# Performance work log

Measured on AMD Instinct MI355X. Metric: run time of the kernel, lower is better.

The kernel has to match this reference:

```python
import jax, jax.numpy as jnp
import numpy as np

CF_ITERS = 5
CF_K = 0.02
DECAY = [0.9, 0.93, 0.85, 0.97, 0.88, 0.94]
N_CHAMBERS = 6
RES_DIM = 100
B = 262144

COUPLING = np.array([
    [0.0, -0.3, 0.6, 0.4, -0.2, 0.3],
    [-0.3, 0.0, -0.5, -0.7, 0.6, 0.4],
    [0.6, -0.5, 0.0, 0.3, -0.3, 0.2],
    [0.4, -0.7, 0.3, 0.0, -0.4, 0.5],
    [-0.2, 0.6, -0.3, -0.4, 0.0, 0.3],
    [0.3, 0.4, 0.2, 0.5, 0.3, 0.0]], dtype=np.float32)


def _init_linear(key, c, fan_out, fan_in):
    kw, kb = jax.random.split(key)
    bound = 1.0 / np.sqrt(fan_in)
    W = jax.random.uniform(kw, (c, fan_out, fan_in), jnp.float32, -bound, bound)
    b = jax.random.uniform(kb, (c, fan_out), jnp.float32, -bound, bound)
    return W, b


def setup_inputs() -> dict:
    key = jax.random.key(0)
    ks = jax.random.split(key, 5)
    res = jax.random.normal(ks[0], (B, RES_DIM), jnp.float32)
    W1, b1 = _init_linear(ks[1], N_CHAMBERS, 128, RES_DIM)
    W2, b2 = _init_linear(ks[2], N_CHAMBERS, 64, 128)
    W3, b3 = _init_linear(ks[3], N_CHAMBERS, 32, 64)
    W4, b4 = _init_linear(ks[4], N_CHAMBERS, 1, 32)
    coupling = jnp.asarray(COUPLING)
    return {"res": res, "W1": W1, "b1": b1, "W2": W2, "b2": b2,
            "W3": W3, "b3": b3, "W4": W4, "b4": b4, "coupling": coupling}


def reference(res, W1, b1, W2, b2, W3, b3, W4, b4, coupling):
    silu = jax.nn.silu
    # batched 6 per-chamber MLPs: [B, C, hidden]
    h = silu(jnp.einsum('bd,chd->bch', res, W1) + b1)      # [B,6,128]
    h = silu(jnp.einsum('bch,coh->bco', h, W2) + b2)       # [B,6,64]
    h = silu(jnp.einsum('bco,cpo->bcp', h, W3) + b3)       # [B,6,32]
    raw = (jnp.einsum('bcp,cqp->bcq', h, W4) + b4)[..., 0]  # [B,6]
    act = jax.nn.sigmoid(raw)
    decay = jnp.asarray(DECAY, dtype=jnp.float32)
    for _ in range(CF_ITERS):
        act = act * decay
        # infl[b,i,j] = CF_K * sin(act[b,j] - act[b,i])
        infl = CF_K * jnp.sin(act[:, None, :] - act[:, :, None])  # [B,6,6]
        act = act + jnp.sum(infl * coupling[None], axis=2)
        act = jnp.clip(act, 0.0, 1.0)
    return (act, raw)
```

## Files before the change

kernel.cpp:

```cpp
#include <hip/hip_runtime.h>


typedef unsigned int u32;
typedef __attribute__((ext_vector_type(8))) short bf16x8;
typedef __attribute__((ext_vector_type(4))) float f32x4;

#define RES_DIM 100
#define NCH 6
#define FRAGS_PER_CH 52
#define NFRAG (NCH*FRAGS_PER_CH)
#define WS_BYTES ((size_t)NFRAG*2048)

#define MFMA16 __builtin_amdgcn_mfma_f32_16x16x32_bf16
#define CFENCE() asm volatile("" ::: "memory")

union FragU { bf16x8 v; u32 u[4]; uint4 q; };

__device__ __forceinline__ void split2(float f0, float f1, u32 &hp, u32 &lp){
    u32 h;
    asm("v_cvt_pk_bf16_f32 %0, %1, %2" : "=v"(h) : "v"(f0), "v"(f1));
    float l0 = f0 - __uint_as_float(h << 16);
    float l1 = f1 - __uint_as_float(h & 0xffff0000u);
    u32 l;
    asm("v_cvt_pk_bf16_f32 %0, %1, %2" : "=v"(l) : "v"(l0), "v"(l1));
    hp = h; lp = l;
}

__device__ __forceinline__ float silu1(float x){
    return x * __builtin_amdgcn_rcpf(1.f + __expf(-x));
}
__device__ __forceinline__ f32x4 silu4(f32x4 v){
    f32x4 r; r[0]=silu1(v[0]); r[1]=silu1(v[1]); r[2]=silu1(v[2]); r[3]=silu1(v[3]); return r;
}
__device__ __forceinline__ float sin_rev(float x){ return __builtin_amdgcn_sinf(x*0.15915494309189535f); }

__device__ __forceinline__ void load_frag(const u32* __restrict__ wsb, int frag, int lane,
                                          bf16x8 &h, bf16x8 &l){
    const uint4* p = (const uint4*)(wsb + ((size_t)frag << 9) + (lane << 3));
    FragU H, L; H.q = p[0]; L.q = p[1];
    h = H.v; l = L.v;
}

__device__ __forceinline__ f32x4 triple(f32x4 acc, bf16x8 ah, bf16x8 al, bf16x8 bh, bf16x8 bl){
    acc = MFMA16(ah, bh, acc, 0, 0, 0);
    acc = MFMA16(al, bh, acc, 0, 0, 0);
    acc = MFMA16(ah, bl, acc, 0, 0, 0);
    return acc;
}

__global__ void __launch_bounds__(256) prep_kernel(
    const float* __restrict__ W1, const float* __restrict__ W2,
    const float* __restrict__ W3, u32* __restrict__ ws)
{
    const int f = blockIdx.x * 4 + (threadIdx.x >> 6);
    const int lane = threadIdx.x & 63;
    const int c = f / FRAGS_PER_CH, r = f % FRAGS_PER_CH;
    const int n15 = lane & 15, quad = lane >> 4;
    float vals[8];
    if (r < 32) {
        int n = r >> 2, k = r & 3;
        const float* wp = W1 + (size_t)c*128*RES_DIM + (size_t)(n*16 + n15)*RES_DIM;
        #pragma unroll
        for (int j=0;j<8;j++){
            int kk = k*32 + quad*8 + j;
            vals[j] = (kk < RES_DIM) ? wp[kk] : 0.f;
        }
    } else if (r < 48) {
        int rr = r - 32; int n = rr >> 2, k = rr & 3;
        const float* wp = W2 + (size_t)c*64*128 + (size_t)(n*16 + n15)*128;
        #pragma unroll
        for (int j=0;j<8;j++) vals[j] = wp[k*32 + quad*8 + j];
    } else {
        int rr = r - 48; int n = rr >> 1, k = rr & 1;
        const float* wp = W3 + (size_t)c*32*64 + (size_t)(n*16 + n15)*64;
        #pragma unroll
        for (int j=0;j<8;j++) vals[j] = wp[k*32 + quad*8 + j];
    }
    u32 hp[4], lp[4];
    #pragma unroll
    for (int i=0;i<4;i++) split2(vals[2*i], vals[2*i+1], hp[i], lp[i]);
    u32* dst = ws + ((size_t)f << 9) + (lane << 3);
    *(uint4*)(dst)     = make_uint4(hp[0],hp[1],hp[2],hp[3]);
    *(uint4*)(dst + 4) = make_uint4(lp[0],lp[1],lp[2],lp[3]);
}

#define TB_STRIDE 36
#define TB_SIZE (32*TB_STRIDE)

__global__ void __launch_bounds__(256, 2) chambers_mfma(
    const float* __restrict__ res, const u32* __restrict__ wsb,
    const float* __restrict__ b1, const float* __restrict__ b2,
    const float* __restrict__ b3, const float* __restrict__ W4,
    const float* __restrict__ b4, const float* __restrict__ Cpl,
    float* __restrict__ out, int nsamp)
{
    __shared__ __align__(16) float tb[4][TB_SIZE];
    __shared__ float rawld[4*32*7];

    const int tid  = threadIdx.x;
    const int w    = tid >> 6, lane = tid & 63;
    const int n15  = lane & 15, quad = lane >> 4;
    const int m_base = (blockIdx.x * 4 + w) * 32;

    bf16x8 rh[2][4], rl[2][4];
    #pragma unroll
    for (int mt=0; mt<2; mt++){
        const float* row = res + (size_t)(m_base + mt*16 + n15) * RES_DIM;
        #pragma unroll
        for (int ks=0; ks<4; ks++){
            float v[8];
            if (ks < 3){
                float4 A = *(const float4*)(row + ks*32 + quad*8);
                float4 B = *(const float4*)(row + ks*32 + quad*8 + 4);
                v[0]=A.x; v[1]=A.y; v[2]=A.z; v[3]=A.w;
                v[4]=B.x; v[5]=B.y; v[6]=B.z; v[7]=B.w;
            } else {
                float4 A = make_float4(0.f,0.f,0.f,0.f);
                if (quad == 0) A = *(const float4*)(row + 96);
                v[0]=A.x; v[1]=A.y; v[2]=A.z; v[3]=A.w;
                v[4]=0.f; v[5]=0.f; v[6]=0.f; v[7]=0.f;
            }
            FragU H, L;
            #pragma unroll
            for (int i=0;i<4;i++) split2(v[2*i], v[2*i+1], H.u[i], L.u[i]);
            rh[mt][ks]=H.v; rl[mt][ks]=L.v;
        }
    }

    for (int c=0; c<NCH; c++){
        const float* b1c = b1 + c*128;
        const float* b2c = b2 + c*64;
        const float* b3c = b3 + c*32;
        const int fbase = c*FRAGS_PER_CH;

        f32x4 c2[2][4];
        #pragma unroll
        for (int mt=0; mt<2; mt++)
            #pragma unroll
            for (int nt=0; nt<4; nt++){
                float bb = b2c[nt*16 + n15];
                f32x4 t = {bb,bb,bb,bb}; c2[mt][nt] = t;
            }

        bf16x8 fh[4], fl[4];
        load_frag(wsb, fbase + 0, lane, fh[0], fl[0]);
        load_frag(wsb, fbase + 1, lane, fh[1], fl[1]);
        load_frag(wsb, fbase + 2, lane, fh[2], fl[2]);
        load_frag(wsb, fbase + 3, lane, fh[3], fl[3]);

        for (int kk=0; kk<4; kk++){
            bf16x8 w2h[4], w2l[4];
            #pragma unroll
            for (int nt=0; nt<4; nt++) load_frag(wsb, fbase + 32 + nt*4 + kk, lane, w2h[nt], w2l[nt]);

            #pragma unroll
            for (int pp=0; pp<2; pp++){
                int p = kk*2 + pp;
                float bb = b1c[p*16 + n15];
                f32x4 z = {0.f,0.f,0.f,0.f};
                f32x4 A0h = {bb,bb,bb,bb}, A0u = z, A0v = z;
                f32x4 A1h = A0h,           A1u = z, A1v = z;
                #pragma unroll
                for (int ks=0; ks<4; ks++){
                    bf16x8 bh = fh[ks], bl = fl[ks];
                    if (p*4 + ks < 28)
                        load_frag(wsb, fbase + p*4 + ks + 4, lane, fh[ks], fl[ks]);
                    A0h = MFMA16(rh[0][ks], bh, A0h, 0,0,0);
                    A1h = MFMA16(rh[1][ks], bh, A1h, 0,0,0);
                    A0u = MFMA16(rl[0][ks], bh, A0u, 0,0,0);
                    A1u = MFMA16(rl[1][ks], bh, A1u, 0,0,0);
                    A0v = MFMA16(rh[0][ks], bl, A0v, 0,0,0);
                    A1v = MFMA16(rh[1][ks], bl, A1v, 0,0,0);
                }
                f32x4 s0 = silu4((A0h + A0u) + A0v);
                f32x4 s1 = silu4((A1h + A1u) + A1v);
                #pragma unroll
                for (int r=0; r<4; r++){
                    tb[w][(quad*4 + r)*TB_STRIDE      + pp*16 + n15] = s0[r];
                    tb[w][(16 + quad*4 + r)*TB_STRIDE + pp*16 + n15] = s1[r];
                }
            }
            CFENCE();
            bf16x8 a2h[2], a2l[2];
            #pragma unroll
            for (int mt=0; mt<2; mt++){
                const float* qp = &tb[w][(mt*16 + n15)*TB_STRIDE + quad*8];
                float4 A = *(const float4*)qp;
                float4 B = *(const float4*)(qp + 4);
                FragU H, L;
                split2(A.x, A.y, H.u[0], L.u[0]);
                split2(A.z, A.w, H.u[1], L.u[1]);
                split2(B.x, B.y, H.u[2], L.u[2]);
                split2(B.z, B.w, H.u[3], L.u[3]);
                a2h[mt]=H.v; a2l[mt]=L.v;
            }
            CFENCE();
            #pragma unroll
            for (int nt=0; nt<4; nt++){
                c2[0][nt] = triple(c2[0][nt], a2h[0], a2l[0], w2h[nt], w2l[nt]);
                c2[1][nt] = triple(c2[1][nt], a2h[1], a2l[1], w2h[nt], w2l[nt]);
            }
        }
        #pragma unroll
        for (int mt=0; mt<2; mt++)
            #pragma unroll
            for (int nt=0; nt<4; nt++) c2[mt][nt] = silu4(c2[mt][nt]);

        f32x4 c3[2][2];
        #pragma unroll
        for (int mt=0; mt<2; mt++)
            #pragma unroll
            for (int nt=0; nt<2; nt++){
                float bb = b3c[nt*16 + n15];
                f32x4 t = {bb,bb,bb,bb}; c3[mt][nt] = t;
            }
        for (int k3=0; k3<2; k3++){
            bf16x8 w3h[2], w3l[2];
            #pragma unroll
            for (int nt=0; nt<2; nt++) load_frag(wsb, fbase + 48 + nt*2 + k3, lane, w3h[nt], w3l[nt]);
            #pragma unroll
            for (int mt=0; mt<2; mt++)
                #pragma unroll
                for (int q2=0; q2<2; q2++)
                    #pragma unroll
                    for (int r=0; r<4; r++)
                        tb[w][(mt*16 + quad*4 + r)*TB_STRIDE + q2*16 + n15] = c2[mt][2*k3+q2][r];
            CFENCE();
            bf16x8 a3h[2], a3l[2];
            #pragma unroll
            for (int mt=0; mt<2; mt++){
                const float* qp = &tb[w][(mt*16 + n15)*TB_STRIDE + quad*8];
                float4 A = *(const float4*)qp;
                float4 B = *(const float4*)(qp + 4);
                FragU H, L;
                split2(A.x, A.y, H.u[0], L.u[0]);
                split2(A.z, A.w, H.u[1], L.u[1]);
                split2(B.x, B.y, H.u[2], L.u[2]);
                split2(B.z, B.w, H.u[3], L.u[3]);
                a3h[mt]=H.v; a3l[mt]=L.v;
            }
            CFENCE();
            #pragma unroll
            for (int nt=0; nt<2; nt++){
                c3[0][nt] = triple(c3[0][nt], a3h[0], a3l[0], w3h[nt], w3l[nt]);
                c3[1][nt] = triple(c3[1][nt], a3h[1], a3l[1], w3h[nt], w3l[nt]);
            }
        }
        #pragma unroll
        for (int mt=0; mt<2; mt++)
            #pragma unroll
            for (int nt=0; nt<2; nt++) c3[mt][nt] = silu4(c3[mt][nt]);

        float w4a = W4[c*32 + n15];
        float w4b = W4[c*32 + 16 + n15];
        float bb4 = b4[c];
        #pragma unroll
        for (int mt=0; mt<2; mt++){
            float t0 = c3[mt][0][0]*w4a + c3[mt][1][0]*w4b;
            float t1 = c3[mt][0][1]*w4a + c3[mt][1][1]*w4b;
            float t2 = c3[mt][0][2]*w4a + c3[mt][1][2]*w4b;
            float t3 = c3[mt][0][3]*w4a + c3[mt][1][3]*w4b;
            #pragma unroll
            for (int off=1; off<16; off<<=1){
                t0 += __shfl_xor(t0, off, 64);
                t1 += __shfl_xor(t1, off, 64);
                t2 += __shfl_xor(t2, off, 64);
                t3 += __shfl_xor(t3, off, 64);
            }
            if (n15 == 0){
                int mb = w*32 + mt*16 + quad*4;
                rawld[(mb+0)*7 + c] = t0 + bb4;
                rawld[(mb+1)*7 + c] = t1 + bb4;
                rawld[(mb+2)*7 + c] = t2 + bb4;
                rawld[(mb+3)*7 + c] = t3 + bb4;
            }
        }
    }
    __threadfence_block();

    const int m = lane & 31;
    float rw[6], a[6];
    #pragma unroll
    for (int j=0;j<6;j++){
        rw[j] = rawld[(w*32 + m)*7 + j];
        a[j]  = __builtin_amdgcn_rcpf(1.f + __expf(-rw[j]));
    }
    const float dec[6] = {0.9f,0.93f,0.85f,0.97f,0.88f,0.94f};
    float C[6][6];
    #pragma unroll
    for (int i=0;i<6;i++)
        #pragma unroll
        for (int j=0;j<6;j++) C[i][j] = Cpl[i*6+j];
    #pragma unroll
    for (int it=0; it<5; it++){
        #pragma unroll
        for (int j=0;j<6;j++) a[j] *= dec[j];
        float nz[6];
        #pragma unroll
        for (int i=0;i<6;i++){
            float sum = 0.f;
            #pragma unroll
            for (int j=0;j<6;j++) sum += sin_rev(a[j]-a[i]) * C[i][j];
            nz[i] = a[i] + 0.02f*sum;
        }
        #pragma unroll
        for (int i=0;i<6;i++) a[i] = fminf(fmaxf(nz[i],0.f),1.f);
    }
    if (lane < 32){
        size_t s = (size_t)m_base + m;
        #pragma unroll
        for (int j=0;j<6;j++) out[s*6 + j] = a[j];
        size_t rb = (size_t)nsamp*6 + s*6;
        #pragma unroll
        for (int j=0;j<6;j++) out[rb + j] = rw[j];
    }
}

__global__ void __launch_bounds__(256, 2) chambers_fb(
    const float* __restrict__ res, const float* __restrict__ W1, const float* __restrict__ b1,
    const float* __restrict__ W2, const float* __restrict__ b2,
    const float* __restrict__ W3, const float* __restrict__ b3,
    const float* __restrict__ W4, const float* __restrict__ b4,
    const float* __restrict__ Cpl, float* __restrict__ out, int nsamp)
{
    __shared__ float w2t[128*64];
    __shared__ float h3buf[256][33];
    __shared__ float rawbuf[256][7];
    const int tid = threadIdx.x;
    const long long s = (long long)blockIdx.x * 256 + tid;
    float rf[RES_DIM];
    {
        const float4* rp = (const float4*)(res + s*RES_DIM);
        #pragma unroll
        for (int i=0;i<25;i++){
            float4 v = rp[i];
            rf[4*i+0]=v.x; rf[4*i+1]=v.y; rf[4*i+2]=v.z; rf[4*i+3]=v.w;
        }
    }
    for (int c=0;c<6;c++){
        __syncthreads();
        {
            const float* w2c = W2 + c*64*128;
            for (int k=tid; k<64*128; k+=256){
                int o = k >> 7, u = k & 127;
                w2t[u*64 + o] = w2c[k];
            }
        }
        __syncthreads();
        const float* w1c = W1 + c*128*RES_DIM;
        const float* b1c = b1 + c*128;
        const float* b2c = b2 + c*64;
        float h2a[64];
        #pragma unroll
        for (int o=0;o<64;o++) h2a[o] = b2c[o];
        for (int u=0; u<128; u+=2){
            const float4* wa = (const float4*)(w1c + u*RES_DIM);
            const float4* wb = wa + 25;
            float a0=0.f,a1=0.f,a2=0.f,a3=0.f;
            #pragma unroll
            for (int i=0;i<25;i++){
                float4 va=wa[i], vb=wb[i];
                a0 = fmaf(va.x, rf[4*i+0], a0); a0 = fmaf(va.y, rf[4*i+1], a0);
                a2 = fmaf(va.z, rf[4*i+2], a2); a2 = fmaf(va.w, rf[4*i+3], a2);
                a1 = fmaf(vb.x, rf[4*i+0], a1); a1 = fmaf(vb.y, rf[4*i+1], a1);
                a3 = fmaf(vb.z, rf[4*i+2], a3); a3 = fmaf(vb.w, rf[4*i+3], a3);
            }
            float hh0 = silu1(a0+a2+b1c[u]);
            float hh1 = silu1(a1+a3+b1c[u+1]);
            const float* wr0 = &w2t[u*64];
            const float* wr1 = &w2t[(u+1)*64];
            #pragma unroll
            for (int o=0;o<64;o+=4){
                float4 va = *(const float4*)(wr0+o);
                float4 vb = *(const float4*)(wr1+o);
                h2a[o+0] = fmaf(va.x, hh0, fmaf(vb.x, hh1, h2a[o+0]));
                h2a[o+1] = fmaf(va.y, hh0, fmaf(vb.y, hh1, h2a[o+1]));
                h2a[o+2] = fmaf(va.z, hh0, fmaf(vb.z, hh1, h2a[o+2]));
                h2a[o+3] = fmaf(va.w, hh0, fmaf(vb.w, hh1, h2a[o+3]));
            }
        }
        #pragma unroll
        for (int o=0;o<64;o++) h2a[o] = silu1(h2a[o]);
        {
            const float* w3c = W3 + c*32*64;
            const float* b3c = b3 + c*32;
            for (int p=0; p<32; p+=2){
                const float4* wa = (const float4*)(w3c + p*64);
                const float4* wb = wa + 16;
                float a0=0.f,a1=0.f,a2=0.f,a3=0.f;
                #pragma unroll
                for (int k=0;k<16;k++){
                    float4 va=wa[k], vb=wb[k];
                    a0 = fmaf(va.x, h2a[4*k+0], a0); a0 = fmaf(va.y, h2a[4*k+1], a0);
                    a2 = fmaf(va.z, h2a[4*k+2], a2); a2 = fmaf(va.w, h2a[4*k+3], a2);
                    a1 = fmaf(vb.x, h2a[4*k+0], a1); a1 = fmaf(vb.y, h2a[4*k+1], a1);
                    a3 = fmaf(vb.z, h2a[4*k+2], a3); a3 = fmaf(vb.w, h2a[4*k+3], a3);
                }
                h3buf[tid][p]   = silu1(a0+a2+b3c[p]);
                h3buf[tid][p+1] = silu1(a1+a3+b3c[p+1]);
            }
        }
        {
            const float4* w4p = (const float4*)(W4 + c*32);
            float a0=0.f, a1=0.f;
            #pragma unroll
            for (int k=0;k<8;k++){
                float4 v = w4p[k];
                a0 = fmaf(v.x, h3buf[tid][4*k+0], a0);
                a1 = fmaf(v.y, h3buf[tid][4*k+1], a1);
                a0 = fmaf(v.z, h3buf[tid][4*k+2], a0);
                a1 = fmaf(v.w, h3buf[tid][4*k+3], a1);
            }
            rawbuf[tid][c] = a0+a1+b4[c];
        }
    }
    float a[6], rw[6];
    #pragma unroll
    for (int j=0;j<6;j++){ rw[j]=rawbuf[tid][j]; a[j]=__builtin_amdgcn_rcpf(1.f+__expf(-rw[j])); }
    const float dec[6] = {0.9f,0.93f,0.85f,0.97f,0.88f,0.94f};
    float C[6][6];
    #pragma unroll
    for (int i=0;i<6;i++)
        #pragma unroll
        for (int j=0;j<6;j++) C[i][j]=Cpl[i*6+j];
    #pragma unroll
    for (int it=0; it<5; it++){
        #pragma unroll
        for (int j=0;j<6;j++) a[j]*=dec[j];
        float nz[6];
        #pragma unroll
        for (int i=0;i<6;i++){
            float sum=0.f;
            #pragma unroll
            for (int j=0;j<6;j++) sum += sin_rev(a[j]-a[i]) * C[i][j];
            nz[i]=a[i]+0.02f*sum;
        }
        #pragma unroll
        for (int i=0;i<6;i++) a[i]=fminf(fmaxf(nz[i],0.f),1.f);
    }
    long long ob = s*6;
    #pragma unroll
    for (int j=0;j<6;j++) out[ob+j] = a[j];
    long long rb = (long long)nsamp*6 + ob;
    #pragma unroll
    for (int j=0;j<6;j++) out[rb+j] = rw[j];
}

extern "C" void kernel_launch(void* const* d_in, const int* in_sizes, int n_in,
                              void* d_out, int out_size, void* d_ws, size_t ws_size,
                              hipStream_t stream) {
    const float* res = (const float*)d_in[0];
    const float* W1  = (const float*)d_in[1];
    const float* b1  = (const float*)d_in[2];
    const float* W2  = (const float*)d_in[3];
    const float* b2  = (const float*)d_in[4];
    const float* W3  = (const float*)d_in[5];
    const float* b3  = (const float*)d_in[6];
    const float* W4  = (const float*)d_in[7];
    const float* b4  = (const float*)d_in[8];
    const float* Cpl = (const float*)d_in[9];
    float* out = (float*)d_out;
    int nsamp = in_sizes[0] / RES_DIM;

    if (ws_size >= WS_BYTES) {
        u32* ws = (u32*)d_ws;
        prep_kernel<<<NFRAG/4, 256, 0, stream>>>(W1, W2, W3, ws);
        chambers_mfma<<<nsamp/128, 256, 0, stream>>>(res, ws, b1, b2, b3, W4, b4, Cpl, out, nsamp);
    } else {
        chambers_fb<<<nsamp/256, 256, 0, stream>>>(res, W1, b1, W2, b2, W3, b3, W4, b4, Cpl, out, nsamp);
    }
}
```

Baseline: 421.3 us.

## Switch layer-1 GEMM to 32x32x16 MFMA with K=112 padding

```diff
diff --git a/kernel.cpp b/kernel.cpp
--- a/kernel.cpp
+++ b/kernel.cpp
@@ -4,14 +4,16 @@
 typedef unsigned int u32;
 typedef __attribute__((ext_vector_type(8))) short bf16x8;
 typedef __attribute__((ext_vector_type(4))) float f32x4;
+typedef __attribute__((ext_vector_type(16))) float f32x16;
 
 #define RES_DIM 100
 #define NCH 6
-#define FRAGS_PER_CH 52
+#define FRAGS_PER_CH 48
 #define NFRAG (NCH*FRAGS_PER_CH)
 #define WS_BYTES ((size_t)NFRAG*2048)
 
 #define MFMA16 __builtin_amdgcn_mfma_f32_16x16x32_bf16
+#define MFMA32 __builtin_amdgcn_mfma_f32_32x32x16_bf16
 #define CFENCE() asm volatile("" ::: "memory")
 
 union FragU { bf16x8 v; u32 u[4]; uint4 q; };
@@ -57,21 +59,22 @@
     const int c = f / FRAGS_PER_CH, r = f % FRAGS_PER_CH;
     const int n15 = lane & 15, quad = lane >> 4;
     float vals[8];
-    if (r < 32) {
-        int n = r >> 2, k = r & 3;
-        const float* wp = W1 + (size_t)c*128*RES_DIM + (size_t)(n*16 + n15)*RES_DIM;
+    if (r < 28) {
+        int nt = r / 7, ks7 = r % 7;
+        const float* wp = W1 + (size_t)c*128*RES_DIM + (size_t)(nt*32 + (lane & 31))*RES_DIM;
+        int kb = ks7*16 + (lane >> 5)*8;
         #pragma unroll
         for (int j=0;j<8;j++){
-            int kk = k*32 + quad*8 + j;
+            int kk = kb + j;
             vals[j] = (kk < RES_DIM) ? wp[kk] : 0.f;
         }
-    } else if (r < 48) {
-        int rr = r - 32; int n = rr >> 2, k = rr & 3;
+    } else if (r < 44) {
+        int rr = r - 28; int n = rr >> 2, k = rr & 3;
         const float* wp = W2 + (size_t)c*64*128 + (size_t)(n*16 + n15)*128;
         #pragma unroll
         for (int j=0;j<8;j++) vals[j] = wp[k*32 + quad*8 + j];
     } else {
-        int rr = r - 48; int n = rr >> 1, k = rr & 1;
+        int rr = r - 44; int n = rr >> 1, k = rr & 1;
         const float* wp = W3 + (size_t)c*32*64 + (size_t)(n*16 + n15)*64;
         #pragma unroll
         for (int j=0;j<8;j++) vals[j] = wp[k*32 + quad*8 + j];
@@ -100,30 +103,31 @@
     const int tid  = threadIdx.x;
     const int w    = tid >> 6, lane = tid & 63;
     const int n15  = lane & 15, quad = lane >> 4;
+    const int n31  = lane & 31, h32 = lane >> 5;
     const int m_base = (blockIdx.x * 4 + w) * 32;
 
-    bf16x8 rh[2][4], rl[2][4];
-    #pragma unroll
-    for (int mt=0; mt<2; mt++){
-        const float* row = res + (size_t)(m_base + mt*16 + n15) * RES_DIM;
-        #pragma unroll
-        for (int ks=0; ks<4; ks++){
+    bf16x8 rAh[7], rAl[7];
+    {
+        const float* row = res + (size_t)(m_base + n31) * RES_DIM;
+        #pragma unroll
+        for (int ks7=0; ks7<7; ks7++){
+            int kb = ks7*16 + h32*8;
             float v[8];
-            if (ks < 3){
-                float4 A = *(const float4*)(row + ks*32 + quad*8);
-                float4 B = *(const float4*)(row + ks*32 + quad*8 + 4);
+            if (ks7 < 6){
+                float4 A = *(const float4*)(row + kb);
+                float4 B = *(const float4*)(row + kb + 4);
                 v[0]=A.x; v[1]=A.y; v[2]=A.z; v[3]=A.w;
                 v[4]=B.x; v[5]=B.y; v[6]=B.z; v[7]=B.w;
             } else {
                 float4 A = make_float4(0.f,0.f,0.f,0.f);
-                if (quad == 0) A = *(const float4*)(row + 96);
+                if (h32 == 0) A = *(const float4*)(row + 96);
                 v[0]=A.x; v[1]=A.y; v[2]=A.z; v[3]=A.w;
                 v[4]=0.f; v[5]=0.f; v[6]=0.f; v[7]=0.f;
             }
             FragU H, L;
             #pragma unroll
             for (int i=0;i<4;i++) split2(v[2*i], v[2*i+1], H.u[i], L.u[i]);
-            rh[mt][ks]=H.v; rl[mt][ks]=L.v;
+            rAh[ks7]=H.v; rAl[ks7]=L.v;
         }
     }
 
@@ -142,43 +146,34 @@
                 f32x4 t = {bb,bb,bb,bb}; c2[mt][nt] = t;
             }
 
-        bf16x8 fh[4], fl[4];
+        bf16x8 fh[2], fl[2];
         load_frag(wsb, fbase + 0, lane, fh[0], fl[0]);
         load_frag(wsb, fbase + 1, lane, fh[1], fl[1]);
-        load_frag(wsb, fbase + 2, lane, fh[2], fl[2]);
-        load_frag(wsb, fbase + 3, lane, fh[3], fl[3]);
-
+
+        #pragma unroll
         for (int kk=0; kk<4; kk++){
             bf16x8 w2h[4], w2l[4];
             #pragma unroll
-            for (int nt=0; nt<4; nt++) load_frag(wsb, fbase + 32 + nt*4 + kk, lane, w2h[nt], w2l[nt]);
-
-            #pragma unroll
-            for (int pp=0; pp<2; pp++){
-                int p = kk*2 + pp;
-                float bb = b1c[p*16 + n15];
-                f32x4 z = {0.f,0.f,0.f,0.f};
-                f32x4 A0h = {bb,bb,bb,bb}, A0u = z, A0v = z;
-                f32x4 A1h = A0h,           A1u = z, A1v = z;
-                #pragma unroll
-                for (int ks=0; ks<4; ks++){
-                    bf16x8 bh = fh[ks], bl = fl[ks];
-                    if (p*4 + ks < 28)
-                        load_frag(wsb, fbase + p*4 + ks + 4, lane, fh[ks], fl[ks]);
-                    A0h = MFMA16(rh[0][ks], bh, A0h, 0,0,0);
-                    A1h = MFMA16(rh[1][ks], bh, A1h, 0,0,0);
-                    A0u = MFMA16(rl[0][ks], bh, A0u, 0,0,0);
-                    A1u = MFMA16(rl[1][ks], bh, A1u, 0,0,0);
-                    A0v = MFMA16(rh[0][ks], bl, A0v, 0,0,0);
-                    A1v = MFMA16(rh[1][ks], bl, A1v, 0,0,0);
-                }
-                f32x4 s0 = silu4((A0h + A0u) + A0v);
-                f32x4 s1 = silu4((A1h + A1u) + A1v);
-                #pragma unroll
-                for (int r=0; r<4; r++){
-                    tb[w][(quad*4 + r)*TB_STRIDE      + pp*16 + n15] = s0[r];
-                    tb[w][(16 + quad*4 + r)*TB_STRIDE + pp*16 + n15] = s1[r];
-                }
+            for (int nt=0; nt<4; nt++) load_frag(wsb, fbase + 28 + nt*4 + kk, lane, w2h[nt], w2l[nt]);
+
+            float bb = b1c[kk*32 + n31];
+            f32x16 Dh, Dc1, Dc2;
+            #pragma unroll
+            for (int i=0;i<16;i++){ Dh[i]=bb; Dc1[i]=0.f; Dc2[i]=0.f; }
+            #pragma unroll
+            for (int ks7=0; ks7<7; ks7++){
+                const int i = kk*7 + ks7;
+                bf16x8 bh = fh[i & 1], bl = fl[i & 1];
+                if (i < 26) load_frag(wsb, fbase + i + 2, lane, fh[i & 1], fl[i & 1]);
+                Dh  = MFMA32(rAh[ks7], bh, Dh,  0,0,0);
+                Dc1 = MFMA32(rAl[ks7], bh, Dc1, 0,0,0);
+                Dc2 = MFMA32(rAh[ks7], bl, Dc2, 0,0,0);
+            }
+            #pragma unroll
+            for (int reg=0; reg<16; reg++){
+                float d = silu1((Dh[reg] + Dc1[reg]) + Dc2[reg]);
+                int m = (reg & 3) + 8*(reg >> 2) + 4*h32;
+                tb[w][m*TB_STRIDE + n31] = d;
             }
             CFENCE();
             bf16x8 a2h[2], a2l[2];
@@ -217,7 +212,7 @@
         for (int k3=0; k3<2; k3++){
             bf16x8 w3h[2], w3l[2];
             #pragma unroll
-            for (int nt=0; nt<2; nt++) load_frag(wsb, fbase + 48 + nt*2 + k3, lane, w3h[nt], w3l[nt]);
+            for (int nt=0; nt<2; nt++) load_frag(wsb, fbase + 44 + nt*2 + k3, lane, w3h[nt], w3l[nt]);
             #pragma unroll
             for (int mt=0; mt<2; mt++)
                 #pragma unroll
```

Measured after the change: 422.5 us. No clear change (+0.3%).
